# Optimization experiments

Hardware: AMD Instinct MI355X
Metric: run time of the kernel (lower is better)

## Reference

```python
import jax, jax.numpy as jnp
import numpy as np

B, S, H, C = 16, 4096, 1024, 64

def setup_inputs() -> dict:
    key = jax.random.key(0)
    k1, k2 = jax.random.split(key)
    hidden = jax.random.normal(k1, (B, S, H), dtype=jnp.float32)
    querys = jax.random.normal(k2, (C, H), dtype=jnp.float32)
    return {"hidden": hidden, "querys": querys}

def reference(hidden, querys):
    # scores: [B, C, S] = einsum over hidden_size
    scores = jnp.einsum('bsh,ch->bcs', hidden, querys)
    # softmax over the sequence axis
    factor = jax.nn.softmax(scores, axis=2)
    # pooled: [B, C, H]
    result = jnp.einsum('bcs,bsh->bch', factor, hidden)
    # flatten to [B, C*H]
    return result.reshape(-1, querys.shape[0] * querys.shape[1])
```

## Files before the change

kernel.cpp:

```cpp
#include <hip/hip_runtime.h>
#include <math.h>

#define BB 16
#define SS 4096
#define HH 1024
#define CC 64

typedef __attribute__((ext_vector_type(4))) float f32x4;
typedef __attribute__((ext_vector_type(8))) short s16x8;

__device__ __forceinline__ ushort f2bf(float x) {
    union { float f; unsigned u; } un; un.f = x;
    unsigned r = (un.u + 0x7FFFu + ((un.u >> 16) & 1u)) >> 16;
    return (ushort)r;
}
__device__ __forceinline__ float bf2f(ushort h) {
    union { unsigned u; float f; } un; un.u = ((unsigned)h) << 16; return un.f;
}

__global__ __launch_bounds__(256) void prep_querys_kernel(
    const float* __restrict__ q, ushort* __restrict__ qhi, ushort* __restrict__ qlo)
{
    const int i4 = blockIdx.x * 256 + threadIdx.x;
    const float4 v = ((const float4*)q)[i4];
    ushort4 h, l;
    h.x = f2bf(v.x); l.x = f2bf(v.x - bf2f(h.x));
    h.y = f2bf(v.y); l.y = f2bf(v.y - bf2f(h.y));
    h.z = f2bf(v.z); l.z = f2bf(v.z - bf2f(h.z));
    h.w = f2bf(v.w); l.w = f2bf(v.w - bf2f(h.w));
    ((ushort4*)qhi)[i4] = h;
    ((ushort4*)qlo)[i4] = l;
}

__global__ __launch_bounds__(256) void scores_kernel(
    const float* __restrict__ hidden, const ushort* __restrict__ qhi,
    const ushort* __restrict__ qlo, float* __restrict__ scores)
{
    const int b = blockIdx.y, t = threadIdx.x;
    const int w = t >> 6, lane = t & 63, col = lane & 15, quad = lane >> 4;
    const int s0 = blockIdx.x * 64 + w * 16;

    const float*  arow = hidden + ((size_t)b * SS + s0 + col) * HH + quad * 8;
    const ushort* qh0  = qhi + (size_t)col * HH + quad * 8;
    const ushort* ql0  = qlo + (size_t)col * HH + quad * 8;

    f32x4 acc[4];
#pragma unroll
    for (int nt = 0; nt < 4; ++nt) acc[nt] = (f32x4){0.f, 0.f, 0.f, 0.f};

    float4 a0 = *(const float4*)arow;
    float4 a1 = *(const float4*)(arow + 4);

    for (int k0 = 0; k0 < HH; k0 += 32) {
        s16x8 bh[4], bl[4];
#pragma unroll
        for (int nt = 0; nt < 4; ++nt) {
            bh[nt] = *(const s16x8*)(qh0 + (size_t)nt * 16 * HH + k0);
            bl[nt] = *(const s16x8*)(ql0 + (size_t)nt * 16 * HH + k0);
        }
        const float af[8] = {a0.x, a0.y, a0.z, a0.w, a1.x, a1.y, a1.z, a1.w};
        s16x8 ah, al;
#pragma unroll
        for (int j = 0; j < 8; ++j) {
            const ushort h = f2bf(af[j]);
            ah[j] = (short)h;
            al[j] = (short)f2bf(af[j] - bf2f(h));
        }
        if (k0 + 32 < HH) {
            a0 = *(const float4*)(arow + k0 + 32);
            a1 = *(const float4*)(arow + k0 + 36);
        }
#pragma unroll
        for (int nt = 0; nt < 4; ++nt) {
            acc[nt] = __builtin_amdgcn_mfma_f32_16x16x32_bf16(ah, bh[nt], acc[nt], 0, 0, 0);
            acc[nt] = __builtin_amdgcn_mfma_f32_16x16x32_bf16(ah, bl[nt], acc[nt], 0, 0, 0);
            acc[nt] = __builtin_amdgcn_mfma_f32_16x16x32_bf16(al, bh[nt], acc[nt], 0, 0, 0);
        }
    }
#pragma unroll
    for (int nt = 0; nt < 4; ++nt) {
        const int c = nt * 16 + col;
        *(f32x4*)&scores[((size_t)(b * CC + c)) * SS + s0 + quad * 4] = acc[nt];
    }
}

__global__ __launch_bounds__(256) void softmax_kernel(
    const float* __restrict__ scores, ushort* __restrict__ factor)
{
    const float* p = scores + (size_t)blockIdx.x * SS;
    ushort* f = factor + (size_t)blockIdx.x * SS;
    const int t = threadIdx.x;
    float4 v[4];
    float m = -3.0e38f;
#pragma unroll
    for (int i = 0; i < 4; ++i) {
        v[i] = *(const float4*)&p[t * 4 + i * 1024];
        m = fmaxf(m, fmaxf(fmaxf(v[i].x, v[i].y), fmaxf(v[i].z, v[i].w)));
    }
#pragma unroll
    for (int off = 1; off < 64; off <<= 1) m = fmaxf(m, __shfl_xor(m, off));
    __shared__ float redm[4];
    __shared__ float reds[4];
    const int wave = t >> 6, lane = t & 63;
    if (lane == 0) redm[wave] = m;
    __syncthreads();
    m = fmaxf(fmaxf(redm[0], redm[1]), fmaxf(redm[2], redm[3]));

    float sum = 0.0f;
#pragma unroll
    for (int i = 0; i < 4; ++i) {
        v[i].x = __expf(v[i].x - m); v[i].y = __expf(v[i].y - m);
        v[i].z = __expf(v[i].z - m); v[i].w = __expf(v[i].w - m);
        sum += (v[i].x + v[i].y) + (v[i].z + v[i].w);
    }
#pragma unroll
    for (int off = 1; off < 64; off <<= 1) sum += __shfl_xor(sum, off);
    if (lane == 0) reds[wave] = sum;
    __syncthreads();
    sum = (reds[0] + reds[1]) + (reds[2] + reds[3]);
    const float inv = 1.0f / sum;
#pragma unroll
    for (int i = 0; i < 4; ++i) {
        ushort4 o;
        o.x = f2bf(v[i].x * inv); o.y = f2bf(v[i].y * inv);
        o.z = f2bf(v[i].z * inv); o.w = f2bf(v[i].w * inv);
        ((ushort4*)f)[t + i * 256] = o;
    }
}

#define KSPLIT 8
__global__ __launch_bounds__(256) void pool_kernel(
    const float* __restrict__ hidden, const ushort* __restrict__ factor,
    float* __restrict__ parts)
{
    __shared__ __align__(16) ushort Ht[64][72];

    const int b  = blockIdx.y;
    const int h0 = blockIdx.x * 64;
    const int ks = blockIdx.z;
    const int sbeg = ks * (SS / KSPLIT);
    const int t = threadIdx.x;
    const int w = t >> 6, lane = t & 63, col = lane & 15, quad = lane >> 4;
    const int hc = t & 15;
    const int sq = t >> 4;

    f32x4 acc[4];
#pragma unroll
    for (int j = 0; j < 4; ++j) acc[j] = (f32x4){0.f, 0.f, 0.f, 0.f};

    const float* hbase = hidden + (size_t)b * SS * HH + h0;
    const ushort* fbase = factor + (size_t)(b * CC + w * 16 + col) * SS + sbeg;

    float v[16];
#pragma unroll
    for (int pp = 0; pp < 2; ++pp)
#pragma unroll
        for (int mm = 0; mm < 4; ++mm)
#pragma unroll
            for (int e = 0; e < 2; ++e)
                v[pp * 8 + mm * 2 + e] =
                    hbase[(size_t)(sbeg + 2 * (sq + 16 * pp) + e) * HH + hc + 16 * mm];

    for (int sc = 0; sc < SS / KSPLIT; sc += 64) {
        __syncthreads();
#pragma unroll
        for (int pp = 0; pp < 2; ++pp)
#pragma unroll
            for (int mm = 0; mm < 4; ++mm) {
                unsigned pack = (unsigned)f2bf(v[pp * 8 + mm * 2 + 0]) |
                                ((unsigned)f2bf(v[pp * 8 + mm * 2 + 1]) << 16);
                ((unsigned*)Ht)[(hc + 16 * mm) * 36 + (sq + 16 * pp)] = pack;
            }
        __syncthreads();

        const s16x8 fa0 = *(const s16x8*)&fbase[sc + quad * 8];
        const s16x8 fa1 = *(const s16x8*)&fbase[sc + 32 + quad * 8];

        if (sc + 64 < SS / KSPLIT) {
#pragma unroll
            for (int pp = 0; pp < 2; ++pp)
#pragma unroll
                for (int mm = 0; mm < 4; ++mm)
#pragma unroll
                    for (int e = 0; e < 2; ++e)
                        v[pp * 8 + mm * 2 + e] =
                            hbase[(size_t)(sbeg + sc + 64 + 2 * (sq + 16 * pp) + e) * HH + hc + 16 * mm];
        }

#pragma unroll
        for (int ksp = 0; ksp < 2; ++ksp) {
            const s16x8 fa = ksp ? fa1 : fa0;
#pragma unroll
            for (int nt = 0; nt < 4; ++nt) {
                const s16x8 hb = *(const s16x8*)&Ht[nt * 16 + col][ksp * 32 + quad * 8];
                acc[nt] = __builtin_amdgcn_mfma_f32_16x16x32_bf16(fa, hb, acc[nt], 0, 0, 0);
            }
        }
    }

    float* dst = parts + (size_t)ks * (BB * CC * HH) + (size_t)b * (CC * HH);
#pragma unroll
    for (int nt = 0; nt < 4; ++nt) {
        const int h = h0 + nt * 16 + col;
#pragma unroll
        for (int r = 0; r < 4; ++r) {
            const int c = w * 16 + quad * 4 + r;
            dst[(size_t)c * HH + h] = acc[nt][r];
        }
    }
}

__global__ __launch_bounds__(256) void reduce8_kernel(
    const float* __restrict__ parts, float* __restrict__ out)
{
    const int i = blockIdx.x * 256 + threadIdx.x;
    const float4* p = (const float4*)parts;
    float4 r = {0.f, 0.f, 0.f, 0.f};
#pragma unroll
    for (int j = 0; j < KSPLIT; ++j) {
        const float4 a = p[i + (size_t)j * 262144];
        r.x += a.x; r.y += a.y; r.z += a.z; r.w += a.w;
    }
    ((float4*)out)[i] = r;
}

extern "C" void kernel_launch(void* const* d_in, const int* in_sizes, int n_in,
                              void* d_out, int out_size, void* d_ws, size_t ws_size,
                              hipStream_t stream)
{
    const float* hidden = (const float*)d_in[0];
    const float* querys = (const float*)d_in[1];
    float* out = (float*)d_out;

    float*  scores = (float*)d_ws;
    ushort* factor = (ushort*)((char*)d_ws + (16u << 20));
    ushort* qhi    = (ushort*)((char*)d_ws + (24u << 20));
    ushort* qlo    = qhi + CC * HH;
    float*  parts  = (float*)((char*)d_ws + (32u << 20));

    prep_querys_kernel<<<dim3(CC * HH / 1024), 256, 0, stream>>>(querys, qhi, qlo);
    scores_kernel<<<dim3(SS / 64, BB), 256, 0, stream>>>(hidden, qhi, qlo, scores);
    softmax_kernel<<<dim3(BB * CC), 256, 0, stream>>>(scores, factor);
    pool_kernel<<<dim3(HH / 64, BB, KSPLIT), 256, 0, stream>>>(hidden, factor, parts);
    reduce8_kernel<<<dim3(1024), 256, 0, stream>>>(parts, out);
}
```

Before: 502.6 us.

## Deepen scores prefetch pipeline and vectorize pool kernel hidden loads

The scores kernel is fully unrolled over K and gains deeper software pipelining: hidden rows are prefetched two iterations ahead with a triple buffer, the qhi fragments one iteration ahead, and the MFMAs are regrouped by operand. It also gets a launch-bounds occupancy hint. The pool kernel now loads hidden as float4 rows instead of scalar strided loads, then transposes into LDS with 16-bit stores. The aim is to hide global load latency and cut the number of load instructions, at the cost of higher register pressure and possible LDS bank conflicts on the narrower stores.

```diff
diff --git a/kernel.cpp b/kernel.cpp
--- a/kernel.cpp
+++ b/kernel.cpp
@@ -32,7 +32,7 @@
     ((ushort4*)qlo)[i4] = l;
 }
 
-__global__ __launch_bounds__(256) void scores_kernel(
+__global__ __launch_bounds__(256, 4) void scores_kernel(
     const float* __restrict__ hidden, const ushort* __restrict__ qhi,
     const ushort* __restrict__ qlo, float* __restrict__ scores)
 {
@@ -48,17 +48,40 @@
 #pragma unroll
     for (int nt = 0; nt < 4; ++nt) acc[nt] = (f32x4){0.f, 0.f, 0.f, 0.f};
 
-    float4 a0 = *(const float4*)arow;
-    float4 a1 = *(const float4*)(arow + 4);
-
-    for (int k0 = 0; k0 < HH; k0 += 32) {
-        s16x8 bh[4], bl[4];
-#pragma unroll
-        for (int nt = 0; nt < 4; ++nt) {
-            bh[nt] = *(const s16x8*)(qh0 + (size_t)nt * 16 * HH + k0);
+    float4 aR[3][2];
+    aR[0][0] = *(const float4*)(arow + 0);
+    aR[0][1] = *(const float4*)(arow + 4);
+    aR[1][0] = *(const float4*)(arow + 32);
+    aR[1][1] = *(const float4*)(arow + 36);
+
+    s16x8 bhR[2][4];
+#pragma unroll
+    for (int nt = 0; nt < 4; ++nt)
+        bhR[0][nt] = *(const s16x8*)(qh0 + (size_t)nt * 16 * HH);
+
+#pragma unroll
+    for (int kk = 0; kk < 32; ++kk) {
+        const int k0 = kk * 32;
+        const int ca = kk % 3;
+        const int cb = kk & 1;
+
+        s16x8 bl[4];
+#pragma unroll
+        for (int nt = 0; nt < 4; ++nt)
             bl[nt] = *(const s16x8*)(ql0 + (size_t)nt * 16 * HH + k0);
-        }
-        const float af[8] = {a0.x, a0.y, a0.z, a0.w, a1.x, a1.y, a1.z, a1.w};
+
+        if (kk + 1 < 32) {
+#pragma unroll
+            for (int nt = 0; nt < 4; ++nt)
+                bhR[cb ^ 1][nt] = *(const s16x8*)(qh0 + (size_t)nt * 16 * HH + k0 + 32);
+        }
+        if (kk + 2 < 32) {
+            aR[(kk + 2) % 3][0] = *(const float4*)(arow + k0 + 64);
+            aR[(kk + 2) % 3][1] = *(const float4*)(arow + k0 + 68);
+        }
+
+        const float af[8] = {aR[ca][0].x, aR[ca][0].y, aR[ca][0].z, aR[ca][0].w,
+                             aR[ca][1].x, aR[ca][1].y, aR[ca][1].z, aR[ca][1].w};
         s16x8 ah, al;
 #pragma unroll
         for (int j = 0; j < 8; ++j) {
@@ -66,17 +89,17 @@
             ah[j] = (short)h;
             al[j] = (short)f2bf(af[j] - bf2f(h));
         }
-        if (k0 + 32 < HH) {
-            a0 = *(const float4*)(arow + k0 + 32);
-            a1 = *(const float4*)(arow + k0 + 36);
-        }
-#pragma unroll
-        for (int nt = 0; nt < 4; ++nt) {
-            acc[nt] = __builtin_amdgcn_mfma_f32_16x16x32_bf16(ah, bh[nt], acc[nt], 0, 0, 0);
+#pragma unroll
+        for (int nt = 0; nt < 4; ++nt)
+            acc[nt] = __builtin_amdgcn_mfma_f32_16x16x32_bf16(ah, bhR[cb][nt], acc[nt], 0, 0, 0);
+#pragma unroll
+        for (int nt = 0; nt < 4; ++nt)
+            acc[nt] = __builtin_amdgcn_mfma_f32_16x16x32_bf16(al, bhR[cb][nt], acc[nt], 0, 0, 0);
+#pragma unroll
+        for (int nt = 0; nt < 4; ++nt)
             acc[nt] = __builtin_amdgcn_mfma_f32_16x16x32_bf16(ah, bl[nt], acc[nt], 0, 0, 0);
-            acc[nt] = __builtin_amdgcn_mfma_f32_16x16x32_bf16(al, bh[nt], acc[nt], 0, 0, 0);
-        }
-    }
+    }
+
 #pragma unroll
     for (int nt = 0; nt < 4; ++nt) {
         const int c = nt * 16 + col;
@@ -141,51 +164,41 @@
     const int sbeg = ks * (SS / KSPLIT);
     const int t = threadIdx.x;
     const int w = t >> 6, lane = t & 63, col = lane & 15, quad = lane >> 4;
-    const int hc = t & 15;
-    const int sq = t >> 4;
+    const int srow = t >> 2;
+    const int hq   = t & 3;
 
     f32x4 acc[4];
 #pragma unroll
     for (int j = 0; j < 4; ++j) acc[j] = (f32x4){0.f, 0.f, 0.f, 0.f};
 
-    const float* hbase = hidden + (size_t)b * SS * HH + h0;
+    const float*  hsrc  = hidden + (size_t)b * SS * HH + h0 + hq * 4;
     const ushort* fbase = factor + (size_t)(b * CC + w * 16 + col) * SS + sbeg;
 
-    float v[16];
-#pragma unroll
-    for (int pp = 0; pp < 2; ++pp)
-#pragma unroll
-        for (int mm = 0; mm < 4; ++mm)
-#pragma unroll
-            for (int e = 0; e < 2; ++e)
-                v[pp * 8 + mm * 2 + e] =
-                    hbase[(size_t)(sbeg + 2 * (sq + 16 * pp) + e) * HH + hc + 16 * mm];
+    float4 g[4];
+#pragma unroll
+    for (int j = 0; j < 4; ++j)
+        g[j] = *(const float4*)&hsrc[(size_t)(sbeg + srow) * HH + j * 16];
 
     for (int sc = 0; sc < SS / KSPLIT; sc += 64) {
         __syncthreads();
 #pragma unroll
-        for (int pp = 0; pp < 2; ++pp)
-#pragma unroll
-            for (int mm = 0; mm < 4; ++mm) {
-                unsigned pack = (unsigned)f2bf(v[pp * 8 + mm * 2 + 0]) |
-                                ((unsigned)f2bf(v[pp * 8 + mm * 2 + 1]) << 16);
-                ((unsigned*)Ht)[(hc + 16 * mm) * 36 + (sq + 16 * pp)] = pack;
-            }
+        for (int j = 0; j < 4; ++j) {
+            const int h = hq * 4 + j * 16;
+            Ht[h + 0][srow] = f2bf(g[j].x);
+            Ht[h + 1][srow] = f2bf(g[j].y);
+            Ht[h + 2][srow] = f2bf(g[j].z);
+            Ht[h + 3][srow] = f2bf(g[j].w);
+        }
         __syncthreads();
+
+        if (sc + 64 < SS / KSPLIT) {
+#pragma unroll
+            for (int j = 0; j < 4; ++j)
+                g[j] = *(const float4*)&hsrc[(size_t)(sbeg + sc + 64 + srow) * HH + j * 16];
+        }
 
         const s16x8 fa0 = *(const s16x8*)&fbase[sc + quad * 8];
         const s16x8 fa1 = *(const s16x8*)&fbase[sc + 32 + quad * 8];
-
-        if (sc + 64 < SS / KSPLIT) {
-#pragma unroll
-            for (int pp = 0; pp < 2; ++pp)
-#pragma unroll
-                for (int mm = 0; mm < 4; ++mm)
-#pragma unroll
-                    for (int e = 0; e < 2; ++e)
-                        v[pp * 8 + mm * 2 + e] =
-                            hbase[(size_t)(sbeg + sc + 64 + 2 * (sq + 16 * pp) + e) * HH + hc + 16 * mm];
-        }
 
 #pragma unroll
         for (int ksp = 0; ksp < 2; ++ksp) {
```

Measured after the change: 509.6 us. No clear change (+1.4%).

## Stage hidden tiles via global_load_lds double buffering in scores and pool kernels

Applied to the files above, without the earlier changes.

Both the scores and pool kernels now copy 64x64 fp32 tiles of hidden straight into XOR-swizzled LDS with global_load_lds, double-buffered so the next tile loads while the current one is consumed. The pool kernel is software-pipelined: it converts the transposed tile to bf16 in one step and runs the MFMAs on the previous tile in the next, which adds an extra iteration and a second barrier. The goal is coalesced 16-byte global loads and fewer live registers than the per-thread strided loads used before. Launch-bound occupancy hints are added, and LDS use grows to 32KB or more per block, which may limit occupancy.

```diff
diff --git a/kernel.cpp b/kernel.cpp
--- a/kernel.cpp
+++ b/kernel.cpp
@@ -5,6 +5,7 @@
 #define SS 4096
 #define HH 1024
 #define CC 64
+#define KSPLIT 8
 
 typedef __attribute__((ext_vector_type(4))) float f32x4;
 typedef __attribute__((ext_vector_type(8))) short s16x8;
@@ -16,6 +17,26 @@
 }
 __device__ __forceinline__ float bf2f(ushort h) {
     union { unsigned u; float f; } un; un.u = ((unsigned)h) << 16; return un.f;
+}
+
+__device__ __forceinline__ void gld_lds16(const float* g, float* l) {
+    __builtin_amdgcn_global_load_lds(
+        (const __attribute__((address_space(1))) void*)g,
+        (__attribute__((address_space(3))) void*)l, 16, 0, 0);
+}
+
+__device__ __forceinline__ void stage64x64(const float* gbase, float* lds, int t) {
+    const int w = t >> 6;
+    const int L = t & 63;
+    const int rsub = L >> 4;
+    const int p = L & 15;
+#pragma unroll
+    for (int i = 0; i < 4; ++i) {
+        const int row = i * 16 + w * 4 + rsub;
+        const int kblk = p ^ (row & 7);
+        gld_lds16(gbase + (size_t)row * HH + kblk * 4,
+                  lds + (size_t)(i * 16 + w * 4) * 64);
+    }
 }
 
 __global__ __launch_bounds__(256) void prep_querys_kernel(
@@ -32,55 +53,65 @@
     ((ushort4*)qlo)[i4] = l;
 }
 
-__global__ __launch_bounds__(256) void scores_kernel(
+__global__ __launch_bounds__(256, 4) void scores_kernel(
     const float* __restrict__ hidden, const ushort* __restrict__ qhi,
     const ushort* __restrict__ qlo, float* __restrict__ scores)
 {
+    __shared__ float Abuf[2][64 * 64];
+
     const int b = blockIdx.y, t = threadIdx.x;
     const int w = t >> 6, lane = t & 63, col = lane & 15, quad = lane >> 4;
-    const int s0 = blockIdx.x * 64 + w * 16;
-
-    const float*  arow = hidden + ((size_t)b * SS + s0 + col) * HH + quad * 8;
-    const ushort* qh0  = qhi + (size_t)col * HH + quad * 8;
-    const ushort* ql0  = qlo + (size_t)col * HH + quad * 8;
+    const int s0 = blockIdx.x * 64;
 
     f32x4 acc[4];
 #pragma unroll
     for (int nt = 0; nt < 4; ++nt) acc[nt] = (f32x4){0.f, 0.f, 0.f, 0.f};
 
-    float4 a0 = *(const float4*)arow;
-    float4 a1 = *(const float4*)(arow + 4);
-
-    for (int k0 = 0; k0 < HH; k0 += 32) {
-        s16x8 bh[4], bl[4];
-#pragma unroll
-        for (int nt = 0; nt < 4; ++nt) {
-            bh[nt] = *(const s16x8*)(qh0 + (size_t)nt * 16 * HH + k0);
-            bl[nt] = *(const s16x8*)(ql0 + (size_t)nt * 16 * HH + k0);
-        }
-        const float af[8] = {a0.x, a0.y, a0.z, a0.w, a1.x, a1.y, a1.z, a1.w};
-        s16x8 ah, al;
-#pragma unroll
-        for (int j = 0; j < 8; ++j) {
-            const ushort h = f2bf(af[j]);
-            ah[j] = (short)h;
-            al[j] = (short)f2bf(af[j] - bf2f(h));
-        }
-        if (k0 + 32 < HH) {
-            a0 = *(const float4*)(arow + k0 + 32);
-            a1 = *(const float4*)(arow + k0 + 36);
-        }
-#pragma unroll
-        for (int nt = 0; nt < 4; ++nt) {
-            acc[nt] = __builtin_amdgcn_mfma_f32_16x16x32_bf16(ah, bh[nt], acc[nt], 0, 0, 0);
-            acc[nt] = __builtin_amdgcn_mfma_f32_16x16x32_bf16(ah, bl[nt], acc[nt], 0, 0, 0);
-            acc[nt] = __builtin_amdgcn_mfma_f32_16x16x32_bf16(al, bh[nt], acc[nt], 0, 0, 0);
+    const float* gA = hidden + ((size_t)b * SS + s0) * HH;
+    stage64x64(gA, Abuf[0], t);
+
+    const int r  = w * 16 + col;
+    const int c7 = col & 7;
+    const ushort* qh0 = qhi + (size_t)col * HH + quad * 8;
+    const ushort* ql0 = qlo + (size_t)col * HH + quad * 8;
+
+    for (int kk = 0; kk < 16; ++kk) {
+        __syncthreads();
+        if (kk + 1 < 16)
+            stage64x64(gA + (kk + 1) * 64, Abuf[(kk + 1) & 1], t);
+        const float* buf = Abuf[kk & 1] + r * 64;
+#pragma unroll
+        for (int ks = 0; ks < 2; ++ks) {
+            const int kg = kk * 64 + ks * 32;
+            s16x8 bh[4], bl[4];
+#pragma unroll
+            for (int nt = 0; nt < 4; ++nt) {
+                bh[nt] = *(const s16x8*)(qh0 + (size_t)nt * 16 * HH + kg);
+                bl[nt] = *(const s16x8*)(ql0 + (size_t)nt * 16 * HH + kg);
+            }
+            const int lb = ks * 8 + quad * 2;
+            const float4 f0 = *(const float4*)(buf + ((lb ^ c7) << 2));
+            const float4 f1 = *(const float4*)(buf + (((lb + 1) ^ c7) << 2));
+            const float af[8] = {f0.x, f0.y, f0.z, f0.w, f1.x, f1.y, f1.z, f1.w};
+            s16x8 ah, al;
+#pragma unroll
+            for (int j = 0; j < 8; ++j) {
+                const ushort h = f2bf(af[j]);
+                ah[j] = (short)h;
+                al[j] = (short)f2bf(af[j] - bf2f(h));
+            }
+#pragma unroll
+            for (int nt = 0; nt < 4; ++nt) {
+                acc[nt] = __builtin_amdgcn_mfma_f32_16x16x32_bf16(ah, bh[nt], acc[nt], 0, 0, 0);
+                acc[nt] = __builtin_amdgcn_mfma_f32_16x16x32_bf16(al, bh[nt], acc[nt], 0, 0, 0);
+                acc[nt] = __builtin_amdgcn_mfma_f32_16x16x32_bf16(ah, bl[nt], acc[nt], 0, 0, 0);
+            }
         }
     }
 #pragma unroll
     for (int nt = 0; nt < 4; ++nt) {
         const int c = nt * 16 + col;
-        *(f32x4*)&scores[((size_t)(b * CC + c)) * SS + s0 + quad * 4] = acc[nt];
+        *(f32x4*)&scores[((size_t)(b * CC + c)) * SS + s0 + w * 16 + quad * 4] = acc[nt];
     }
 }
 
@@ -128,72 +159,70 @@
     }
 }
 
-#define KSPLIT 8
-__global__ __launch_bounds__(256) void pool_kernel(
+__global__ __launch_bounds__(256, 3) void pool_kernel(
     const float* __restrict__ hidden, const ushort* __restrict__ factor,
     float* __restrict__ parts)
 {
+    __shared__ float Sbuf[2][64 * 64];
     __shared__ __align__(16) ushort Ht[64][72];
 
-    const int b  = blockIdx.y;
-    const int h0 = blockIdx.x * 64;
-    const int ks = blockIdx.z;
+    const int b = blockIdx.y, h0 = blockIdx.x * 64, ks = blockIdx.z;
     const int sbeg = ks * (SS / KSPLIT);
     const int t = threadIdx.x;
     const int w = t >> 6, lane = t & 63, col = lane & 15, quad = lane >> 4;
-    const int hc = t & 15;
-    const int sq = t >> 4;
+    const int hT = t & 31;
+    const int sblk = t >> 5;
 
     f32x4 acc[4];
 #pragma unroll
     for (int j = 0; j < 4; ++j) acc[j] = (f32x4){0.f, 0.f, 0.f, 0.f};
 
-    const float* hbase = hidden + (size_t)b * SS * HH + h0;
+    const float*  gH    = hidden + ((size_t)b * SS + sbeg) * HH + h0;
     const ushort* fbase = factor + (size_t)(b * CC + w * 16 + col) * SS + sbeg;
 
-    float v[16];
-#pragma unroll
-    for (int pp = 0; pp < 2; ++pp)
-#pragma unroll
-        for (int mm = 0; mm < 4; ++mm)
-#pragma unroll
-            for (int e = 0; e < 2; ++e)
-                v[pp * 8 + mm * 2 + e] =
-                    hbase[(size_t)(sbeg + 2 * (sq + 16 * pp) + e) * HH + hc + 16 * mm];
-
-    for (int sc = 0; sc < SS / KSPLIT; sc += 64) {
+    stage64x64(gH, Sbuf[0], t);
+
+    for (int ci = 0; ci <= 8; ++ci) {
         __syncthreads();
-#pragma unroll
-        for (int pp = 0; pp < 2; ++pp)
-#pragma unroll
-            for (int mm = 0; mm < 4; ++mm) {
-                unsigned pack = (unsigned)f2bf(v[pp * 8 + mm * 2 + 0]) |
-                                ((unsigned)f2bf(v[pp * 8 + mm * 2 + 1]) << 16);
-                ((unsigned*)Ht)[(hc + 16 * mm) * 36 + (sq + 16 * pp)] = pack;
-            }
+        if (ci + 1 <= 7)
+            stage64x64(gH + (size_t)(ci + 1) * 64 * HH, Sbuf[(ci + 1) & 1], t);
+
+        float vals[16];
+        if (ci <= 7) {
+            const float* sb = Sbuf[ci & 1];
+#pragma unroll
+            for (int u = 0; u < 2; ++u) {
+                const int h = hT + 32 * u;
+#pragma unroll
+                for (int i = 0; i < 8; ++i) {
+                    const int s = sblk * 8 + i;
+                    vals[u * 8 + i] = sb[s * 64 + ((((h >> 2) ^ i) << 2) | (h & 3))];
+                }
+            }
+        }
+        if (ci >= 1) {
+            const int so = (ci - 1) * 64;
+            const s16x8 fa0 = *(const s16x8*)&fbase[so + quad * 8];
+            const s16x8 fa1 = *(const s16x8*)&fbase[so + 32 + quad * 8];
+#pragma unroll
+            for (int ksp = 0; ksp < 2; ++ksp) {
+                const s16x8 fa = ksp ? fa1 : fa0;
+#pragma unroll
+                for (int nt = 0; nt < 4; ++nt) {
+                    const s16x8 hb = *(const s16x8*)&Ht[nt * 16 + col][ksp * 32 + quad * 8];
+                    acc[nt] = __builtin_amdgcn_mfma_f32_16x16x32_bf16(fa, hb, acc[nt], 0, 0, 0);
+                }
+            }
+        }
         __syncthreads();
-
-        const s16x8 fa0 = *(const s16x8*)&fbase[sc + quad * 8];
-        const s16x8 fa1 = *(const s16x8*)&fbase[sc + 32 + quad * 8];
-
-        if (sc + 64 < SS / KSPLIT) {
-#pragma unroll
-            for (int pp = 0; pp < 2; ++pp)
-#pragma unroll
-                for (int mm = 0; mm < 4; ++mm)
-#pragma unroll
-                    for (int e = 0; e < 2; ++e)
-                        v[pp * 8 + mm * 2 + e] =
-                            hbase[(size_t)(sbeg + sc + 64 + 2 * (sq + 16 * pp) + e) * HH + hc + 16 * mm];
-        }
-
-#pragma unroll
-        for (int ksp = 0; ksp < 2; ++ksp) {
-            const s16x8 fa = ksp ? fa1 : fa0;
-#pragma unroll
-            for (int nt = 0; nt < 4; ++nt) {
-                const s16x8 hb = *(const s16x8*)&Ht[nt * 16 + col][ksp * 32 + quad * 8];
-                acc[nt] = __builtin_amdgcn_mfma_f32_16x16x32_bf16(fa, hb, acc[nt], 0, 0, 0);
+        if (ci <= 7) {
+#pragma unroll
+            for (int u = 0; u < 2; ++u) {
+                const int h = hT + 32 * u;
+                s16x8 pk;
+#pragma unroll
+                for (int i = 0; i < 8; ++i) pk[i] = (short)f2bf(vals[u * 8 + i]);
+                *(s16x8*)&Ht[h][sblk * 8] = pk;
             }
         }
     }
```

New measurement: 493.1 us. No clear change (-1.9%).
